# Kernel optimization log

Measured on AMD Instinct MI355X. Metric: run time of the kernel, lower is better.

## Reference

```python
import jax, jax.numpy as jnp
import numpy as np

D_MODEL = 1024
NUM_HEADS = 16
D_K = D_MODEL // NUM_HEADS


def setup_inputs() -> dict:
    key = jax.random.key(0)
    ks = jax.random.split(key, 12)
    B, L, D = 1, 4096, D_MODEL
    s = 1.0 / np.sqrt(D)
    return {
        "q": jax.random.normal(ks[0], (B, L, D), jnp.float32),
        "k": jax.random.normal(ks[1], (B, L, D), jnp.float32),
        "v": jax.random.normal(ks[2], (B, L, D), jnp.float32),
        "wq": jax.random.normal(ks[3], (D, D), jnp.float32) * s,
        "bq": jnp.zeros((D,), jnp.float32),
        "wk": jax.random.normal(ks[4], (D, D), jnp.float32) * s,
        "bk": jnp.zeros((D,), jnp.float32),
        "wv": jax.random.normal(ks[5], (D, D), jnp.float32) * s,
        "bv": jnp.zeros((D,), jnp.float32),
        "wo": jax.random.normal(ks[6], (D, D), jnp.float32) * s,
        "bo": jnp.zeros((D,), jnp.float32),
    }


def reference(q, k, v, wq, bq, wk, bk, wv, bv, wo, bo):
    B, L, D = q.shape
    H, dk = NUM_HEADS, D_K
    # linear projections then split heads: [B, L, D] -> [B, H, L, dk]
    def proj(x, w, b):
        return (x @ w.T + b).reshape(B, L, H, dk).transpose(0, 2, 1, 3)
    qh = proj(q, wq, bq)
    kh = proj(k, wk, bk)
    vh = proj(v, wv, bv)
    scores = jnp.einsum("bhqd,bhkd->bhqk", qh, kh) / jnp.sqrt(jnp.float32(dk))
    attn = jax.nn.softmax(scores, axis=-1)  # [B, H, L, L]
    out = jnp.einsum("bhqk,bhkd->bhqd", attn, vh)
    out = out.transpose(0, 2, 1, 3).reshape(B, L, D)
    return out @ wo.T + bo
```

## Files before the change

kernel.cpp:

```cpp
#include <hip/hip_runtime.h>
#include <hip/hip_bf16.h>
#include <stdint.h>


typedef __bf16 bf16_t;
typedef __bf16 bf16x8 __attribute__((ext_vector_type(8)));
typedef __bf16 bf16x4 __attribute__((ext_vector_type(4)));
typedef float f32x4 __attribute__((ext_vector_type(4)));
typedef unsigned short u16x8 __attribute__((ext_vector_type(8)));

#define MFMA_BF16 __builtin_amdgcn_mfma_f32_16x16x32_bf16

__device__ __forceinline__ void async_copy16(const void* g, void* lds) {
  __builtin_amdgcn_global_load_lds(
      (__attribute__((address_space(1))) void*)(uintptr_t)g,
      (__attribute__((address_space(3))) void*)lds, 16, 0, 0);
}

__global__ __launch_bounds__(256) void cast_f32_bf16(
    const float* __restrict__ s0, bf16_t* __restrict__ d0, int n0,
    const float* __restrict__ s1, bf16_t* __restrict__ d1, int n1,
    const float* __restrict__ s2, bf16_t* __restrict__ d2, int n2,
    const float* __restrict__ s3, bf16_t* __restrict__ d3, int n3,
    const float* __restrict__ s4, bf16_t* __restrict__ d4, int n4,
    const float* __restrict__ s5, bf16_t* __restrict__ d5, int n5,
    const float* __restrict__ s6, bf16_t* __restrict__ d6, int n6) {
  const float* s;
  bf16_t* d;
  int n;
  switch (blockIdx.z) {
    case 0: s = s0; d = d0; n = n0; break;
    case 1: s = s1; d = d1; n = n1; break;
    case 2: s = s2; d = d2; n = n2; break;
    case 3: s = s3; d = d3; n = n3; break;
    case 4: s = s4; d = d4; n = n4; break;
    case 5: s = s5; d = d5; n = n5; break;
    default: s = s6; d = d6; n = n6; break;
  }
  const int i = (blockIdx.x * 256 + threadIdx.x) * 8;
  if (i >= n) return;
  float4 a = *(const float4*)(s + i);
  float4 b = *(const float4*)(s + i + 4);
  bf16x8 o;
  o[0] = (bf16_t)a.x; o[1] = (bf16_t)a.y; o[2] = (bf16_t)a.z; o[3] = (bf16_t)a.w;
  o[4] = (bf16_t)b.x; o[5] = (bf16_t)b.y; o[6] = (bf16_t)b.z; o[7] = (bf16_t)b.w;
  *(bf16x8*)(d + i) = o;
}

template <typename CT>
__global__ __launch_bounds__(256) void gemm3_bt(
    const bf16_t* __restrict__ A0, const bf16_t* __restrict__ W0,
    const float* __restrict__ b0, CT* __restrict__ C0,
    const bf16_t* __restrict__ A1, const bf16_t* __restrict__ W1,
    const float* __restrict__ b1, CT* __restrict__ C1,
    const bf16_t* __restrict__ A2, const bf16_t* __restrict__ W2,
    const float* __restrict__ b2, CT* __restrict__ C2,
    int M, int N, int K) {
  const bf16_t *A, *W;
  const float* bias;
  CT* C;
  if (blockIdx.z == 0)      { A = A0; W = W0; bias = b0; C = C0; }
  else if (blockIdx.z == 1) { A = A1; W = W1; bias = b1; C = C1; }
  else                      { A = A2; W = W2; bias = b2; C = C2; }

  __shared__ bf16_t As[128][32];
  __shared__ bf16_t Bs[128][32];

  const int t = threadIdx.x;
  const int w = t >> 6, lane = t & 63;
  const int quad = lane >> 4, l16 = lane & 15;
  const int wr = w >> 1, wc = w & 1;
  const int m0 = blockIdx.x * 128;
  const int n0 = blockIdx.y * 128;
  const int srow = lane >> 2;
  const int scol = (lane & 3) * 8;

  f32x4 acc[4][4] = {};

  for (int k0 = 0; k0 < K; k0 += 32) {
    async_copy16(&A[(size_t)(m0 + (2 * w) * 16 + srow) * K + k0 + scol],
                 (char*)As + (2 * w) * 1024);
    async_copy16(&A[(size_t)(m0 + (2 * w + 1) * 16 + srow) * K + k0 + scol],
                 (char*)As + (2 * w + 1) * 1024);
    async_copy16(&W[(size_t)(n0 + (2 * w) * 16 + srow) * K + k0 + scol],
                 (char*)Bs + (2 * w) * 1024);
    async_copy16(&W[(size_t)(n0 + (2 * w + 1) * 16 + srow) * K + k0 + scol],
                 (char*)Bs + (2 * w + 1) * 1024);
    __syncthreads();

    bf16x8 af[4], bfr[4];
#pragma unroll
    for (int mt = 0; mt < 4; mt++)
      af[mt] = *(const bf16x8*)&As[wr * 64 + mt * 16 + l16][quad * 8];
#pragma unroll
    for (int nt = 0; nt < 4; nt++)
      bfr[nt] = *(const bf16x8*)&Bs[wc * 64 + nt * 16 + l16][quad * 8];
#pragma unroll
    for (int mt = 0; mt < 4; mt++)
#pragma unroll
      for (int nt = 0; nt < 4; nt++)
        acc[mt][nt] = MFMA_BF16(af[mt], bfr[nt], acc[mt][nt], 0, 0, 0);
    __syncthreads();
  }

#pragma unroll
  for (int nt = 0; nt < 4; nt++) {
    const int col = n0 + wc * 64 + nt * 16 + l16;
    const float bb = bias[col];
#pragma unroll
    for (int mt = 0; mt < 4; mt++) {
#pragma unroll
      for (int r = 0; r < 4; r++) {
        const int row = m0 + wr * 64 + mt * 16 + quad * 4 + r;
        C[(size_t)row * N + col] = (CT)(acc[mt][nt][r] + bb);
      }
    }
  }
}

__global__ __launch_bounds__(256) void frag_tile(
    const bf16_t* __restrict__ s0, bf16_t* __restrict__ d0,
    const bf16_t* __restrict__ s1, bf16_t* __restrict__ d1,
    const bf16_t* __restrict__ s2, bf16_t* __restrict__ d2) {
  const bf16_t* src;
  bf16_t* dst;
  const int z = blockIdx.z;
  if (z == 0)      { src = s0; dst = d0; }
  else if (z == 1) { src = s1; dst = d1; }
  else             { src = s2; dst = d2; }

  const int h = blockIdx.y;
  const int l0 = blockIdx.x * 64;
  const int t = threadIdx.x;

  __shared__ ushort Ts[64][72];

#pragma unroll
  for (int p = 0; p < 2; p++) {
    const int r = p * 32 + (t >> 3);
    const int c = (t & 7) * 8;
    float4 v = *(const float4*)(src + (size_t)(l0 + r) * 1024 + h * 64 + c);
    *(float4*)&Ts[r][c] = v;
  }
  __syncthreads();

  if (z < 2) {
    const float qscale = 0.125f * 1.44269504088896340736f;
#pragma unroll
    for (int p = 0; p < 2; p++) {
      const int gi = p * 256 + t;
      const int l16 = gi & 15, quad = (gi >> 4) & 3, kc = (gi >> 6) & 1;
      const int tl = gi >> 7;
      float4 v = *(const float4*)&Ts[tl * 16 + l16][kc * 32 + quad * 8];
      if (z == 0) {
        bf16x8 b = *(bf16x8*)&v;
#pragma unroll
        for (int e = 0; e < 8; e++) b[e] = (bf16_t)((float)b[e] * qscale);
        v = *(float4*)&b;
      }
      *(float4*)(dst + (size_t)(h * 256 + (l0 >> 4) + tl) * 1024 +
                 (size_t)(kc * 64 + quad * 16 + l16) * 8) = v;
    }
  } else {
#pragma unroll
    for (int p = 0; p < 2; p++) {
      const int gi = p * 256 + t;
      const int l16 = gi & 15, quad = (gi >> 4) & 3, kvc = (gi >> 6) & 1;
      const int dkt = gi >> 7;
      u16x8 tmp;
#pragma unroll
      for (int e = 0; e < 8; e++)
        tmp[e] = Ts[kvc * 32 + quad * 8 + e][dkt * 16 + l16];
      *(u16x8*)(dst + (size_t)(h * 256 + (l0 >> 6) * 4 + dkt) * 1024 +
                (size_t)(kvc * 64 + quad * 16 + l16) * 8) = tmp;
    }
  }
}

__global__ __launch_bounds__(512, 4) void flash_attn(
    const bf16_t* __restrict__ Qt, const bf16_t* __restrict__ Kt,
    const bf16_t* __restrict__ Vt, bf16_t* __restrict__ O, int L) {
  const int i = blockIdx.x;
  const int xcd = i & 7;
  const int slot = i >> 3;
  const int h = xcd * 2 + (slot >> 5);
  const int qblk = slot & 31;

  const int t = threadIdx.x;
  const int w = t >> 6, lane = t & 63;
  const int quad = lane >> 4, l16 = lane & 15;
  const int tq0 = qblk * 8 + w;

  __shared__ bf16_t Kst[2][4096];
  __shared__ bf16_t Vst[2][4096];
  __shared__ bf16_t Pb[8][16][72];

  const size_t hb = (size_t)h * 256 * 1024;

  bf16x8 qa[2];
#pragma unroll
  for (int kc = 0; kc < 2; kc++)
    qa[kc] = *(const bf16x8*)(Qt + hb + (size_t)tq0 * 1024 + kc * 512 +
                              lane * 8);

#define STAGE(it_, buf_)                                                     \
  {                                                                          \
    const size_t cb = hb + (size_t)(it_) * 4096;                             \
    async_copy16(Kt + cb + (size_t)t * 8, (char*)&Kst[buf_][0] + w * 1024);  \
    async_copy16(Vt + cb + (size_t)t * 8, (char*)&Vst[buf_][0] + w * 1024);  \
  }

  STAGE(0, 0);

  f32x4 oT[4] = {};
  float ls = 0.f;

  const int NIT = L / 64;
  for (int it = 0; it < NIT; it++) {
    const int buf = it & 1;
    __syncthreads();
    if (it + 1 < NIT) STAGE(it + 1, buf ^ 1);

    bf16x8 kb[4][2], vb[4][2];
#pragma unroll
    for (int tt = 0; tt < 4; tt++)
#pragma unroll
      for (int kc = 0; kc < 2; kc++)
        kb[tt][kc] = *(const bf16x8*)((const char*)&Kst[buf][0] + tt * 2048 +
                                      kc * 1024 + lane * 16);
#pragma unroll
    for (int dkt = 0; dkt < 4; dkt++)
#pragma unroll
      for (int kvc = 0; kvc < 2; kvc++)
        vb[dkt][kvc] = *(const bf16x8*)((const char*)&Vst[buf][0] +
                                        dkt * 2048 + kvc * 1024 + lane * 16);

    f32x4 sT[4];
#pragma unroll
    for (int tt = 0; tt < 4; tt++) {
      f32x4 z = {0.f, 0.f, 0.f, 0.f};
      z = MFMA_BF16(kb[tt][0], qa[0], z, 0, 0, 0);
      z = MFMA_BF16(kb[tt][1], qa[1], z, 0, 0, 0);
      sT[tt] = z;
    }
#pragma unroll
    for (int tt = 0; tt < 4; tt++) {
      bf16x4 pk;
      float rs = 0.f;
#pragma unroll
      for (int r = 0; r < 4; r++) {
        const float p = __builtin_amdgcn_exp2f(sT[tt][r]);
        rs += p;
        pk[r] = (bf16_t)p;
      }
      ls += rs;
      *(bf16x4*)&Pb[w][l16][tt * 16 + quad * 4] = pk;
    }

    const bf16x8 pf0 = *(const bf16x8*)&Pb[w][l16][quad * 8];
    const bf16x8 pf1 = *(const bf16x8*)&Pb[w][l16][32 + quad * 8];
#pragma unroll
    for (int dkt = 0; dkt < 4; dkt++) {
      oT[dkt] = MFMA_BF16(vb[dkt][0], pf0, oT[dkt], 0, 0, 0);
      oT[dkt] = MFMA_BF16(vb[dkt][1], pf1, oT[dkt], 0, 0, 0);
    }
  }
#undef STAGE

  float l = ls;
  l += __shfl_xor(l, 16);
  l += __shfl_xor(l, 32);
  const float inv = 1.0f / l;
  const size_t row = (size_t)tq0 * 16 + l16;
#pragma unroll
  for (int dkt = 0; dkt < 4; dkt++)
#pragma unroll
    for (int r = 0; r < 4; r++)
      O[row * 1024 + h * 64 + dkt * 16 + quad * 4 + r] =
          (bf16_t)(oT[dkt][r] * inv);
}

extern "C" void kernel_launch(void* const* d_in, const int* in_sizes, int n_in,
                              void* d_out, int out_size, void* d_ws,
                              size_t ws_size, hipStream_t stream) {
  const float* q  = (const float*)d_in[0];
  const float* k  = (const float*)d_in[1];
  const float* v  = (const float*)d_in[2];
  const float* wq = (const float*)d_in[3];
  const float* bq = (const float*)d_in[4];
  const float* wk = (const float*)d_in[5];
  const float* bk = (const float*)d_in[6];
  const float* wv = (const float*)d_in[7];
  const float* bv = (const float*)d_in[8];
  const float* wo = (const float*)d_in[9];
  const float* bo = (const float*)d_in[10];
  float* out = (float*)d_out;

  const int L = 4096, D = 1024;
  const int nLD = L * D;
  const int nDD = D * D;
  bf16_t* p = (bf16_t*)d_ws;
  bf16_t* qb  = p; p += nLD;
  bf16_t* kb  = p; p += nLD;
  bf16_t* vb  = p; p += nLD;
  bf16_t* wqb = p; p += nDD;
  bf16_t* wkb = p; p += nDD;
  bf16_t* wvb = p; p += nDD;
  bf16_t* wob = p; p += nDD;
  bf16_t* Qp  = p; p += nLD;
  bf16_t* Kp  = p; p += nLD;
  bf16_t* Vp  = p; p += nLD;
  bf16_t* Qt  = p; p += nLD;
  bf16_t* Kt  = p; p += nLD;
  bf16_t* Vt  = p; p += nLD;
  bf16_t* Op  = Qp;

  dim3 blk(256);
  cast_f32_bf16<<<dim3(nLD / (256 * 8), 1, 7), blk, 0, stream>>>(
      q, qb, nLD, k, kb, nLD, v, vb, nLD, wq, wqb, nDD, wk, wkb, nDD,
      wv, wvb, nDD, wo, wob, nDD);
  gemm3_bt<bf16_t><<<dim3(L / 128, D / 128, 3), blk, 0, stream>>>(
      qb, wqb, bq, Qp, kb, wkb, bk, Kp, vb, wvb, bv, Vp, L, D, D);
  frag_tile<<<dim3(L / 64, 16, 3), blk, 0, stream>>>(Qp, Qt, Kp, Kt, Vp, Vt);
  flash_attn<<<dim3((L / 128) * 16), dim3(512), 0, stream>>>(Qt, Kt, Vt, Op, L);
  gemm3_bt<float><<<dim3(L / 128, D / 128, 1), blk, 0, stream>>>(
      Op, wob, bo, out, Op, wob, bo, out, Op, wob, bo, out, L, D, D);
}
```

Measured before the change: 271.5 us.

## Split KV range across two wave groups per block and swizzle P buffer

Each attention block now handles 4 query tiles instead of 8, and the two groups of four waves each process half of every 128-key chunk. The partial outputs and row sums are combined through LDS at the end. This doubles the grid size to improve occupancy and latency hiding. The P staging buffer is XOR-swizzled with no padding to avoid LDS bank conflicts. The cost is twice the LDS for K/V staging, an extra reduction step with two barriers, and K/V traffic per query that is twice as high overall.

```diff
diff --git a/kernel.cpp b/kernel.cpp
--- a/kernel.cpp
+++ b/kernel.cpp
@@ -181,59 +181,69 @@
     const bf16_t* __restrict__ Qt, const bf16_t* __restrict__ Kt,
     const bf16_t* __restrict__ Vt, bf16_t* __restrict__ O, int L) {
   const int i = blockIdx.x;
-  const int xcd = i & 7;
   const int slot = i >> 3;
-  const int h = xcd * 2 + (slot >> 5);
-  const int qblk = slot & 31;
+  const int h = (i & 7) * 2 + (slot >> 6);
+  const int qblk = slot & 63;
 
   const int t = threadIdx.x;
   const int w = t >> 6, lane = t & 63;
   const int quad = lane >> 4, l16 = lane & 15;
-  const int tq0 = qblk * 8 + w;
-
-  __shared__ bf16_t Kst[2][4096];
-  __shared__ bf16_t Vst[2][4096];
-  __shared__ bf16_t Pb[8][16][72];
+  const int g = w >> 2;
+  const int ws = w & 3;
+  const int tq = qblk * 4 + ws;
+
+  __shared__ bf16_t Kst[2][8192];
+  __shared__ bf16_t Vst[2][8192];
+  __shared__ bf16_t Pb[8][16][64];
 
   const size_t hb = (size_t)h * 256 * 1024;
 
   bf16x8 qa[2];
 #pragma unroll
   for (int kc = 0; kc < 2; kc++)
-    qa[kc] = *(const bf16x8*)(Qt + hb + (size_t)tq0 * 1024 + kc * 512 +
+    qa[kc] = *(const bf16x8*)(Qt + hb + (size_t)tq * 1024 + kc * 512 +
                               lane * 8);
 
-#define STAGE(it_, buf_)                                                     \
-  {                                                                          \
-    const size_t cb = hb + (size_t)(it_) * 4096;                             \
-    async_copy16(Kt + cb + (size_t)t * 8, (char*)&Kst[buf_][0] + w * 1024);  \
-    async_copy16(Vt + cb + (size_t)t * 8, (char*)&Vst[buf_][0] + w * 1024);  \
+#define STAGE(mc_, buf_)                                                      \
+  {                                                                           \
+    const size_t pb_ = hb + (size_t)(mc_) * 8192;                             \
+    async_copy16(Kt + pb_ + (size_t)t * 8, (char*)&Kst[buf_][0] + w * 1024);  \
+    async_copy16(Kt + pb_ + 4096 + (size_t)t * 8,                             \
+                 (char*)&Kst[buf_][0] + 8192 + w * 1024);                     \
+    async_copy16(Vt + pb_ + (size_t)t * 8, (char*)&Vst[buf_][0] + w * 1024);  \
+    async_copy16(Vt + pb_ + 4096 + (size_t)t * 8,                             \
+                 (char*)&Vst[buf_][0] + 8192 + w * 1024);                     \
   }
 
   STAGE(0, 0);
 
   f32x4 oT[4] = {};
   float ls = 0.f;
-
-  const int NIT = L / 64;
-  for (int it = 0; it < NIT; it++) {
-    const int buf = it & 1;
+  const int swz = (l16 & 7) << 4;
+  char* prow = (char*)&Pb[w][l16][0];
+
+  const int NMC = L / 128;
+  for (int mc = 0; mc < NMC; mc++) {
+    const int buf = mc & 1;
     __syncthreads();
-    if (it + 1 < NIT) STAGE(it + 1, buf ^ 1);
+    if (mc + 1 < NMC) STAGE(mc + 1, buf ^ 1);
+
+    const char* Kc = (const char*)&Kst[buf][0] + g * 8192;
+    const char* Vc = (const char*)&Vst[buf][0] + g * 8192;
 
     bf16x8 kb[4][2], vb[4][2];
 #pragma unroll
     for (int tt = 0; tt < 4; tt++)
 #pragma unroll
       for (int kc = 0; kc < 2; kc++)
-        kb[tt][kc] = *(const bf16x8*)((const char*)&Kst[buf][0] + tt * 2048 +
-                                      kc * 1024 + lane * 16);
+        kb[tt][kc] =
+            *(const bf16x8*)(Kc + tt * 2048 + kc * 1024 + lane * 16);
 #pragma unroll
     for (int dkt = 0; dkt < 4; dkt++)
 #pragma unroll
       for (int kvc = 0; kvc < 2; kvc++)
-        vb[dkt][kvc] = *(const bf16x8*)((const char*)&Vst[buf][0] +
-                                        dkt * 2048 + kvc * 1024 + lane * 16);
+        vb[dkt][kvc] =
+            *(const bf16x8*)(Vc + dkt * 2048 + kvc * 1024 + lane * 16);
 
     f32x4 sT[4];
 #pragma unroll
@@ -254,11 +264,11 @@
         pk[r] = (bf16_t)p;
       }
       ls += rs;
-      *(bf16x4*)&Pb[w][l16][tt * 16 + quad * 4] = pk;
-    }
-
-    const bf16x8 pf0 = *(const bf16x8*)&Pb[w][l16][quad * 8];
-    const bf16x8 pf1 = *(const bf16x8*)&Pb[w][l16][32 + quad * 8];
+      *(bf16x4*)(prow + ((tt * 32 + quad * 8) ^ swz)) = pk;
+    }
+
+    const bf16x8 pf0 = *(const bf16x8*)(prow + ((quad * 16) ^ swz));
+    const bf16x8 pf1 = *(const bf16x8*)(prow + ((64 + quad * 16) ^ swz));
 #pragma unroll
     for (int dkt = 0; dkt < 4; dkt++) {
       oT[dkt] = MFMA_BF16(vb[dkt][0], pf0, oT[dkt], 0, 0, 0);
@@ -267,17 +277,33 @@
   }
 #undef STAGE
 
-  float l = ls;
-  l += __shfl_xor(l, 16);
-  l += __shfl_xor(l, 32);
-  const float inv = 1.0f / l;
-  const size_t row = (size_t)tq0 * 16 + l16;
-#pragma unroll
-  for (int dkt = 0; dkt < 4; dkt++)
-#pragma unroll
-    for (int r = 0; r < 4; r++)
-      O[row * 1024 + h * 64 + dkt * 16 + quad * 4 + r] =
-          (bf16_t)(oT[dkt][r] * inv);
+  __syncthreads();
+  float* scratch = (float*)&Kst[0][0];
+  if (g == 1) {
+    float* s = scratch + (size_t)(ws * 64 + lane) * 20;
+#pragma unroll
+    for (int dkt = 0; dkt < 4; dkt++) *(f32x4*)(s + dkt * 4) = oT[dkt];
+    s[16] = ls;
+  }
+  __syncthreads();
+  if (g == 0) {
+    const float* s = scratch + (size_t)(ws * 64 + lane) * 20;
+#pragma unroll
+    for (int dkt = 0; dkt < 4; dkt++) oT[dkt] += *(const f32x4*)(s + dkt * 4);
+    ls += s[16];
+
+    float l = ls;
+    l += __shfl_xor(l, 16);
+    l += __shfl_xor(l, 32);
+    const float inv = 1.0f / l;
+    const size_t row = (size_t)tq * 16 + l16;
+#pragma unroll
+    for (int dkt = 0; dkt < 4; dkt++)
+#pragma unroll
+      for (int r = 0; r < 4; r++)
+        O[row * 1024 + h * 64 + dkt * 16 + quad * 4 + r] =
+            (bf16_t)(oT[dkt][r] * inv);
+  }
 }
 
 extern "C" void kernel_launch(void* const* d_in, const int* in_sizes, int n_in,
@@ -322,7 +348,7 @@
   gemm3_bt<bf16_t><<<dim3(L / 128, D / 128, 3), blk, 0, stream>>>(
       qb, wqb, bq, Qp, kb, wkb, bk, Kp, vb, wvb, bv, Vp, L, D, D);
   frag_tile<<<dim3(L / 64, 16, 3), blk, 0, stream>>>(Qp, Qt, Kp, Kt, Vp, Vt);
-  flash_attn<<<dim3((L / 128) * 16), dim3(512), 0, stream>>>(Qt, Kt, Vt, Op, L);
+  flash_attn<<<dim3((L / 64) * 16), dim3(512), 0, stream>>>(Qt, Kt, Vt, Op, L);
   gemm3_bt<float><<<dim3(L / 128, D / 128, 1), blk, 0, stream>>>(
       Op, wob, bo, out, Op, wob, bo, out, Op, wob, bo, out, L, D, D);
 }
```

New measurement: 283.3 us. 1.04x slower.
